# Kernel tuning notes

Hardware: AMD Instinct MI355X
Metric: run time of the kernel (lower is better)

## Reference

```python
import jax, jax.numpy as jnp
import numpy as np

SPATIAL = ((100, 134), (50, 67), (25, 34), (13, 17))
LEN = sum(h * w for h, w in SPATIAL)   # 17821
D, H, L, P = 384, 8, 4, 4
DH = D // H                            # 48
U = D // 3                             # unit_dim = 128
EPS = 1e-5


def _ln(x, g, b):
    m = jnp.mean(x, -1, keepdims=True)
    v = jnp.mean((x - m) ** 2, -1, keepdims=True)
    return (x - m) * jax.lax.rsqrt(v + EPS) * g + b


def _ffn(t, w1, b1, w2, b2, g, b):
    t2 = jax.nn.relu(t @ w1.T + b1) @ w2.T + b2
    return _ln(t + t2, g, b)


def _msda_core(value, loc, attn):
    # value [B,Lv,H,DH]; loc [B,Lq,H,L,P,2] normalized to [0,1]; attn [B,Lq,H,L,P]
    B = value.shape[0]
    Lq = loc.shape[1]
    out = jnp.zeros((B, H, Lq, DH), value.dtype)
    start = 0
    for lvl, (Hl, Wl) in enumerate(SPATIAL):
        n = Hl * Wl
        v = value[:, start:start + n].transpose(0, 2, 1, 3)        # [B,H,n,DH]
        # grid_sample(align_corners=False) semantics: pixel coord = loc*W - 0.5
        x = loc[:, :, :, lvl, :, 0] * Wl - 0.5                      # [B,Lq,H,P]
        y = loc[:, :, :, lvl, :, 1] * Hl - 0.5
        x0 = jnp.floor(x); y0 = jnp.floor(y)
        dx = x - x0; dy = y - y0
        x0i = x0.astype(jnp.int32); y0i = y0.astype(jnp.int32)
        acc = jnp.zeros((B, H, Lq, P, DH), value.dtype)
        corners = ((0, 0, (1 - dx) * (1 - dy)), (1, 0, dx * (1 - dy)),
                   (0, 1, (1 - dx) * dy), (1, 1, dx * dy))
        for ox, oy, w in corners:
            xi = x0i + ox; yi = y0i + oy
            valid = ((xi >= 0) & (xi < Wl) & (yi >= 0) & (yi < Hl)).astype(value.dtype)
            idx = jnp.clip(yi, 0, Hl - 1) * Wl + jnp.clip(xi, 0, Wl - 1)
            idx_t = idx.transpose(0, 2, 1, 3).reshape(B, H, Lq * P)
            g = jnp.take_along_axis(v, idx_t[..., None], axis=2).reshape(B, H, Lq, P, DH)
            acc = acc + g * (w * valid).transpose(0, 2, 1, 3)[..., None]
        out = out + (acc * attn[:, :, :, lvl].transpose(0, 2, 1, 3)[..., None]).sum(axis=3)
        start += n
    return out.transpose(0, 2, 1, 3).reshape(B, Lq, D)


def setup_inputs() -> dict:
    key = jax.random.key(0)
    ks = jax.random.split(key, 16)
    rn = lambda k, s, sc=1.0: jax.random.normal(k, s, jnp.float32) * sc
    inp = {}
    inp['src'] = rn(ks[0], (1, LEN, D))
    inp['space_query'] = rn(ks[1], (1, 1, 2 * U))
    inp['chann_query'] = rn(ks[2], (1, 1, 2 * U))
    inp['pos'] = rn(ks[3], (1, LEN, D))
    inp['reference_points'] = jax.random.uniform(ks[4], (1, LEN, L, 2), jnp.float32)
    inp['spatial_shapes'] = jnp.array(SPATIAL, jnp.int32)
    starts = np.cumsum([0] + [h * w for h, w in SPATIAL[:-1]])
    inp['level_start_index'] = jnp.array(starts, jnp.int32)
    inp['padding_mask'] = jnp.zeros((1, LEN), bool)
    # MSDeformAttn params (torch Linear convention: W is [out_features, in_features])
    inp['W_off'] = rn(ks[5], (H * L * P * 2, D), 0.01)
    inp['b_off'] = rn(ks[6], (H * L * P * 2,), 0.1)
    inp['W_attn'] = rn(ks[7], (H * L * P, D), D ** -0.5)
    inp['b_attn'] = jnp.zeros((H * L * P,), jnp.float32)
    inp['W_val'] = rn(ks[8], (D, D), D ** -0.5)
    inp['b_val'] = jnp.zeros((D,), jnp.float32)
    inp['W_out'] = rn(ks[9], (D, D), D ** -0.5)
    inp['b_out'] = jnp.zeros((D,), jnp.float32)
    # norm1_xy / norm1_zd
    inp['g1xy'] = jnp.ones((2 * U,), jnp.float32); inp['b1xy'] = jnp.zeros((2 * U,), jnp.float32)
    inp['g1zd'] = jnp.ones((U,), jnp.float32); inp['b1zd'] = jnp.zeros((U,), jnp.float32)
    # ffn_xy: Linear(2U,2U) -> relu -> Linear(2U,2U), residual + LN
    inp['fxy_w1'] = rn(ks[10], (2 * U, 2 * U), (2 * U) ** -0.5); inp['fxy_b1'] = jnp.zeros((2 * U,), jnp.float32)
    inp['fxy_w2'] = rn(ks[11], (2 * U, 2 * U), (2 * U) ** -0.5); inp['fxy_b2'] = jnp.zeros((2 * U,), jnp.float32)
    inp['fxy_g'] = jnp.ones((2 * U,), jnp.float32); inp['fxy_b'] = jnp.zeros((2 * U,), jnp.float32)
    # ffn_zd: Linear(U,U) -> relu -> Linear(U,U), residual + LN
    inp['fzd_w1'] = rn(ks[12], (U, U), U ** -0.5); inp['fzd_b1'] = jnp.zeros((U,), jnp.float32)
    inp['fzd_w2'] = rn(ks[13], (U, U), U ** -0.5); inp['fzd_b2'] = jnp.zeros((U,), jnp.float32)
    inp['fzd_g'] = jnp.ones((U,), jnp.float32); inp['fzd_b'] = jnp.zeros((U,), jnp.float32)
    return inp


def reference(src, space_query, chann_query, pos, reference_points, spatial_shapes,
              level_start_index, padding_mask,
              W_off, b_off, W_attn, b_attn, W_val, b_val, W_out, b_out,
              g1xy, b1xy, g1zd, b1zd,
              fxy_w1, fxy_b1, fxy_w2, fxy_b2, fxy_g, fxy_b,
              fzd_w1, fzd_b1, fzd_w2, fzd_b2, fzd_g, fzd_b):
    B, Lq, _ = src.shape
    q = src + pos                                        # with_pos_embed
    value = src @ W_val.T + b_val
    value = jnp.where(padding_mask[..., None], 0.0, value).reshape(B, Lq, H, DH)
    off = (q @ W_off.T + b_off).reshape(B, Lq, H, L, P, 2)
    attn = jax.nn.softmax((q @ W_attn.T + b_attn).reshape(B, Lq, H, L * P), -1)
    attn = attn.reshape(B, Lq, H, L, P)
    wh = jnp.array([[w, h] for h, w in SPATIAL], src.dtype)         # [L,2] as (W,H)
    loc = reference_points[:, :, None, :, None, :] + off / wh[None, None, None, :, None, :]
    src2 = _msda_core(value, loc, attn) @ W_out.T + b_out
    src_xy = _ln(src[..., :2 * U] + src2[..., :2 * U], g1xy, b1xy)
    src_zd = _ln(src[..., 2 * U:] + src2[..., 2 * U:], g1zd, b1zd)
    src_xy = _ffn(src_xy, fxy_w1, fxy_b1, fxy_w2, fxy_b2, fxy_g, fxy_b)
    src_zd = _ffn(src_zd, fzd_w1, fzd_b1, fzd_w2, fzd_b2, fzd_g, fzd_b)
    return jnp.concatenate([src_xy, src_zd], axis=-1)
```

## Files before the change

### kernel.cpp

```cpp
#include <hip/hip_runtime.h>
#include <math.h>

#define LEN 17821
#define DMODEL 384
#define NHEAD 8
#define DHEAD 48
#define WSZ (384 * 384)

typedef float floatx4 __attribute__((ext_vector_type(4)));
typedef short shortx8 __attribute__((ext_vector_type(8)));
typedef unsigned short ushort;

__device__ inline ushort f2bf(float f) {
    unsigned int u = __float_as_uint(f);
    u += 0x7FFFu + ((u >> 16) & 1u);
    return (ushort)(u >> 16);
}
__device__ inline float bf2f(ushort s) {
    return __uint_as_float(((unsigned int)s) << 16);
}

__device__ inline floatx4 mfma_bf16(shortx8 a, shortx8 b, floatx4 c) {
    return __builtin_amdgcn_mfma_f32_16x16x32_bf16(a, b, c, 0, 0, 0);
}

__global__ __launch_bounds__(256)
void prep_w(const float* __restrict__ Wval, const float* __restrict__ Woff,
            const float* __restrict__ Wattn, const float* __restrict__ Wout,
            const float* __restrict__ w1xy, const float* __restrict__ w1zd,
            const float* __restrict__ w2xy, const float* __restrict__ w2zd,
            ushort* __restrict__ wv, ushort* __restrict__ woa,
            ushort* __restrict__ wo, ushort* __restrict__ w1b,
            ushort* __restrict__ w2b) {
    int idx = blockIdx.x * 256 + threadIdx.x;
    if (idx >= WSZ) return;
    int job = blockIdx.y;
    float v; ushort* dst;
    if (job <= 1) {
        int n = idx / 384, k = idx - n * 384;
        if (job == 0) { v = Wval[idx]; dst = wv; }
        else {
            v = n < 256 ? Woff[n * 384 + k] : Wattn[(n - 256) * 384 + k];
            dst = woa;
        }
    } else {
        int e = idx & 7;
        int lane = (idx >> 3) & 63;
        int t = idx >> 9;
        int j = t % 6;
        int t2 = t / 6;
        int wv4 = t2 & 3;
        int ks = t2 >> 2;
        int l15 = lane & 15, quad = lane >> 4;
        int row = wv4 * 96 + j * 16 + l15;
        int k = ks * 32 + quad * 8 + e;
        if (job == 2) { v = Wout[row * 384 + k]; dst = wo; }
        else if (job == 3) {
            v = row < 256 ? (k < 256 ? w1xy[row * 256 + k] : 0.f)
                          : (k >= 256 ? w1zd[(row - 256) * 128 + (k - 256)] : 0.f);
            dst = w1b;
        } else {
            v = row < 256 ? (k < 256 ? w2xy[row * 256 + k] : 0.f)
                          : (k >= 256 ? w2zd[(row - 256) * 128 + (k - 256)] : 0.f);
            dst = w2b;
        }
    }
    dst[idx] = f2bf(v);
}

__global__ __launch_bounds__(384)
void prep_b(const float* __restrict__ boff, const float* __restrict__ battn,
            const float* __restrict__ b1xy, const float* __restrict__ b1zd,
            const float* __restrict__ b2xy, const float* __restrict__ b2zd,
            const float* __restrict__ g1xy, const float* __restrict__ be1xy,
            const float* __restrict__ g1zd, const float* __restrict__ be1zd,
            const float* __restrict__ g2xy, const float* __restrict__ be2xy,
            const float* __restrict__ g2zd, const float* __restrict__ be2zd,
            float* __restrict__ boa, float* __restrict__ b1c,
            float* __restrict__ b2c, float* __restrict__ l1g,
            float* __restrict__ l1b, float* __restrict__ l2g,
            float* __restrict__ l2b) {
    int i = threadIdx.x;
    bool lo = i < 256; int j = lo ? i : i - 256;
    boa[i] = lo ? boff[i] : battn[j];
    b1c[i] = lo ? b1xy[i] : b1zd[j];
    b2c[i] = lo ? b2xy[i] : b2zd[j];
    l1g[i] = lo ? g1xy[i] : g1zd[j];
    l1b[i] = lo ? be1xy[i] : be1zd[j];
    l2g[i] = lo ? g2xy[i] : g2zd[j];
    l2b[i] = lo ? be2xy[i] : be2zd[j];
}

__global__ __launch_bounds__(256)
void cvt_add(const float* __restrict__ src, const float* __restrict__ pos,
             ushort* __restrict__ src_bf, ushort* __restrict__ q_bf, int n8) {
    int i = blockIdx.x * 256 + threadIdx.x;
    if (i >= n8) return;
    float4 s0 = ((const float4*)src)[i * 2], s1 = ((const float4*)src)[i * 2 + 1];
    float4 p0 = ((const float4*)pos)[i * 2], p1 = ((const float4*)pos)[i * 2 + 1];
    shortx8 sb, qb;
    sb[0] = f2bf(s0.x); sb[1] = f2bf(s0.y); sb[2] = f2bf(s0.z); sb[3] = f2bf(s0.w);
    sb[4] = f2bf(s1.x); sb[5] = f2bf(s1.y); sb[6] = f2bf(s1.z); sb[7] = f2bf(s1.w);
    qb[0] = f2bf(s0.x + p0.x); qb[1] = f2bf(s0.y + p0.y);
    qb[2] = f2bf(s0.z + p0.z); qb[3] = f2bf(s0.w + p0.w);
    qb[4] = f2bf(s1.x + p1.x); qb[5] = f2bf(s1.y + p1.y);
    qb[6] = f2bf(s1.z + p1.z); qb[7] = f2bf(s1.w + p1.w);
    ((shortx8*)src_bf)[i] = sb;
    ((shortx8*)q_bf)[i] = qb;
}

#define TSV 128
#define LSTRIDE 40

__global__ __launch_bounds__(256)
void vq_gemm(const ushort* __restrict__ sbq, const ushort* __restrict__ qbq,
             const ushort* __restrict__ wv, const ushort* __restrict__ woa,
             const float* __restrict__ bval, const float* __restrict__ boa,
             ushort* __restrict__ vout, float* __restrict__ oaout) {
    __shared__ ushort As[TSV * LSTRIDE];
    __shared__ ushort Ws[TSV * LSTRIDE];
    bool job = blockIdx.x >= 3;
    int bx = job ? blockIdx.x - 3 : blockIdx.x;
    const ushort* A = job ? qbq : sbq;
    const ushort* W = job ? woa : wv;
    const float* bias = job ? boa : bval;
    int tid = threadIdx.x;
    int lane = tid & 63, wave = tid >> 6;
    int wr = (wave >> 1) * 64, wc = (wave & 1) * 64;
    int l15 = lane & 15, quad = lane >> 4;
    int srow = tid >> 1, shalf = tid & 1;
    int by = blockIdx.y;
    int garow = by * TSV + srow;
    bool avalid = garow < LEN;
    const ushort* ap = A + (size_t)(avalid ? garow : 0) * 384 + shalf * 16;
    const ushort* wp = W + (size_t)(bx * TSV + srow) * 384 + shalf * 16;
    ushort* as_dst = &As[srow * LSTRIDE + shalf * 16];
    ushort* ws_dst = &Ws[srow * LSTRIDE + shalf * 16];

    floatx4 acc[4][4];
    #pragma unroll
    for (int i = 0; i < 4; ++i)
        #pragma unroll
        for (int j = 0; j < 4; ++j)
            acc[i][j] = (floatx4){0.f, 0.f, 0.f, 0.f};

    shortx8 a0 = *(const shortx8*)(ap);
    shortx8 a1 = *(const shortx8*)(ap + 8);
    shortx8 w0 = *(const shortx8*)(wp);
    shortx8 w1 = *(const shortx8*)(wp + 8);

    for (int k0 = 0; k0 < 384; k0 += 32) {
        __syncthreads();
        *(shortx8*)(as_dst + 0) = a0;
        *(shortx8*)(as_dst + 8) = a1;
        *(shortx8*)(ws_dst + 0) = w0;
        *(shortx8*)(ws_dst + 8) = w1;
        __syncthreads();
        if (k0 + 32 < 384) {
            a0 = *(const shortx8*)(ap + k0 + 32);
            a1 = *(const shortx8*)(ap + k0 + 40);
            w0 = *(const shortx8*)(wp + k0 + 32);
            w1 = *(const shortx8*)(wp + k0 + 40);
        }
        shortx8 af[4], bfr[4];
        #pragma unroll
        for (int i = 0; i < 4; ++i)
            af[i] = *(shortx8*)&As[(wr + i * 16 + l15) * LSTRIDE + quad * 8];
        #pragma unroll
        for (int j = 0; j < 4; ++j)
            bfr[j] = *(shortx8*)&Ws[(wc + j * 16 + l15) * LSTRIDE + quad * 8];
        #pragma unroll
        for (int i = 0; i < 4; ++i)
            #pragma unroll
            for (int j = 0; j < 4; ++j)
                acc[i][j] = __builtin_amdgcn_mfma_f32_16x16x32_bf16(
                    af[i], bfr[j], acc[i][j], 0, 0, 0);
    }

    #pragma unroll
    for (int j = 0; j < 4; ++j) {
        int col = bx * TSV + wc + j * 16 + l15;
        float bv = bias[col];
        #pragma unroll
        for (int i = 0; i < 4; ++i) {
            #pragma unroll
            for (int r = 0; r < 4; ++r) {
                int row = by * TSV + wr + i * 16 + quad * 4 + r;
                if (row < LEN) {
                    float v = acc[i][j][r] + bv;
                    if (job) oaout[(size_t)row * 384 + col] = v;
                    else     vout[(size_t)row * 384 + col] = f2bf(v);
                }
            }
        }
    }
}

#define MTOK 8
__global__ __launch_bounds__(384)
void msda_v3(const ushort* __restrict__ value,
             const float* __restrict__ offattn,
             const float* __restrict__ refpts,
             ushort* __restrict__ out) {
    __shared__ int   sx0[MTOK * 128], sy0[MTOK * 128];
    __shared__ float sdx[MTOK * 128], sdy[MTOK * 128], saw[MTOK * 128];
    constexpr int Wi[4]  = {134, 67, 34, 17};
    constexpr int Hi[4]  = {100, 50, 25, 13};
    constexpr int STi[4] = {0, 13400, 16750, 17600};
    int t0 = blockIdx.x * MTOK;
    int tid = threadIdx.x;

    if (tid < MTOK * 8) {
        int ti = tid >> 3, h = tid & 7, t = t0 + ti;
        if (t < LEN) {
            const float* lg = offattn + (size_t)t * 384 + 256 + h * 16;
            float w[16], mx = -3.4e38f;
            #pragma unroll
            for (int s = 0; s < 16; ++s) { w[s] = lg[s]; mx = fmaxf(mx, w[s]); }
            float sum = 0.f;
            #pragma unroll
            for (int s = 0; s < 16; ++s) { w[s] = __expf(w[s] - mx); sum += w[s]; }
            float inv = 1.0f / sum;
            #pragma unroll
            for (int s = 0; s < 16; ++s) saw[ti * 128 + h * 16 + s] = w[s] * inv;
        }
    }
    for (int idx = tid; idx < MTOK * 128; idx += 384) {
        int ti = idx >> 7, rem = idx & 127, h = rem >> 4, p = rem & 15;
        int lvl = p >> 2, pp = p & 3;
        int t = t0 + ti;
        if (t < LEN) {
            float Wl = (float)Wi[lvl], Hl = (float)Hi[lvl];
            const float* op = offattn + (size_t)t * 384 + h * 32 + lvl * 8 + pp * 2;
            float ox = op[0], oy = op[1];
            float rx = refpts[(size_t)t * 8 + lvl * 2];
            float ry = refpts[(size_t)t * 8 + lvl * 2 + 1];
            float x = rx * Wl + ox - 0.5f;
            float y = ry * Hl + oy - 0.5f;
            float x0 = floorf(x), y0 = floorf(y);
            sx0[idx] = (int)x0; sy0[idx] = (int)y0;
            sdx[idx] = x - x0;  sdy[idx] = y - y0;
        }
    }
    __syncthreads();

    int ti = tid / 48;
    int r = tid - ti * 48;
    int h = r / 6;
    int c = r - h * 6;
    int t = t0 + ti;
    if (t >= LEN) return;
    const ushort* vb = value + h * DHEAD + c * 8;
    float a[8] = {};
    #pragma unroll
    for (int p = 0; p < 16; ++p) {
        const int lvl = p >> 2;
        const int Wl = Wi[lvl], Hl = Hi[lvl], st = STi[lvl];
        int base = ti * 128 + h * 16 + p;
        int x0 = sx0[base], y0 = sy0[base];
        float dx = sdx[base], dy = sdy[base], aw = saw[base];
        float cwv[4] = {(1.f - dx) * (1.f - dy), dx * (1.f - dy),
                        (1.f - dx) * dy, dx * dy};
        #pragma unroll
        for (int c2 = 0; c2 < 4; ++c2) {
            int xi = x0 + (c2 & 1), yi = y0 + (c2 >> 1);
            bool valid = (xi >= 0) & (xi < Wl) & (yi >= 0) & (yi < Hl);
            int xc = min(max(xi, 0), Wl - 1);
            int yc = min(max(yi, 0), Hl - 1);
            float s = valid ? aw * cwv[c2] : 0.f;
            shortx8 g = *(const shortx8*)(vb + (size_t)(st + yc * Wl + xc) * 384);
            #pragma unroll
            for (int k = 0; k < 8; ++k) a[k] += s * bf2f(g[k]);
        }
    }
    shortx8 o;
    #pragma unroll
    for (int k = 0; k < 8; ++k) o[k] = f2bf(a[k]);
    *(shortx8*)(out + (size_t)t * 384 + h * DHEAD + c * 8) = o;
}

#define MT 32
#define CST 392

#define GEMM384(WPTR)                                                         \
  {                                                                           \
    const ushort* wp_ = (WPTR) + wave * 3072 + lane * 8;                      \
    _Pragma("unroll")                                                         \
    for (int i_ = 0; i_ < 2; ++i_)                                            \
      _Pragma("unroll")                                                       \
      for (int j_ = 0; j_ < 6; ++j_) acc[i_][j_] = (floatx4){0.f,0.f,0.f,0.f};\
    shortx8 wcr[6][2], wnr[6][2];                                             \
    _Pragma("unroll")                                                         \
    for (int j_ = 0; j_ < 6; ++j_) {                                          \
      wcr[j_][0] = *(const shortx8*)(wp_ + j_ * 512);                         \
      wcr[j_][1] = *(const shortx8*)(wp_ + 12288 + j_ * 512);                 \
    }                                                                         \
    _Pragma("unroll")                                                         \
    for (int ks = 0; ks < 6; ++ks) {                                          \
      if (ks < 5) {                                                           \
        _Pragma("unroll")                                                     \
        for (int j_ = 0; j_ < 6; ++j_) {                                      \
          wnr[j_][0] = *(const shortx8*)(wp_ + (ks*2+2)*12288 + j_*512);      \
          wnr[j_][1] = *(const shortx8*)(wp_ + (ks*2+3)*12288 + j_*512);      \
        }                                                                     \
      }                                                                       \
      const int k0 = ks * 64;                                                 \
      shortx8 a0[2], a1[2];                                                   \
      a0[0] = *(shortx8*)&Cbuf[l15 * CST + k0 + quad * 8];                    \
      a0[1] = *(shortx8*)&Cbuf[l15 * CST + k0 + 32 + quad * 8];               \
      a1[0] = *(shortx8*)&Cbuf[(16 + l15) * CST + k0 + quad * 8];             \
      a1[1] = *(shortx8*)&Cbuf[(16 + l15) * CST + k0 + 32 + quad * 8];        \
      _Pragma("unroll")                                                       \
      for (int sk = 0; sk < 2; ++sk)                                          \
        _Pragma("unroll")                                                     \
        for (int j_ = 0; j_ < 6; ++j_) {                                      \
          acc[0][j_] = mfma_bf16(a0[sk], wcr[j_][sk], acc[0][j_]);            \
          acc[1][j_] = mfma_bf16(a1[sk], wcr[j_][sk], acc[1][j_]);            \
        }                                                                     \
      if (ks < 5) {                                                           \
        _Pragma("unroll")                                                     \
        for (int j_ = 0; j_ < 6; ++j_) {                                      \
          wcr[j_][0] = wnr[j_][0]; wcr[j_][1] = wnr[j_][1];                   \
        }                                                                     \
      }                                                                       \
    }                                                                         \
  }

__global__ __launch_bounds__(256, 4)
void mega_kernel(const ushort* __restrict__ Amsda, const float* __restrict__ src,
                 const ushort* __restrict__ Wo, const ushort* __restrict__ W1,
                 const ushort* __restrict__ W2,
                 const float* __restrict__ bo, const float* __restrict__ b1c,
                 const float* __restrict__ b2c,
                 const float* __restrict__ l1g, const float* __restrict__ l1b,
                 const float* __restrict__ l2g, const float* __restrict__ l2b,
                 float* __restrict__ h1f, float* __restrict__ outp) {
    __shared__ __align__(16) ushort Cbuf[MT * CST];
    __shared__ __align__(16) floatx4 pst4[MT * 8];
    __shared__ __align__(16) floatx4 lnf[MT];

    int tid = threadIdx.x;
    int lane = tid & 63, wave = tid >> 6;
    int l15 = lane & 15, quad = lane >> 4;
    int wcol = wave * 96;
    int by0 = blockIdx.x * MT;

    floatx4 acc[2][6];

    #pragma unroll
    for (int cix = 0; cix < 6; ++cix) {
        int idx = cix * 256 + tid;
        int row = idx / 48, c = idx - row * 48;
        int gr = min(by0 + row, LEN - 1);
        *(shortx8*)(Cbuf + row * CST + c * 8) =
            *(const shortx8*)(Amsda + (size_t)gr * 384 + c * 8);
    }
    __syncthreads();

    GEMM384(Wo);
    __syncthreads();

    #pragma unroll
    for (int j = 0; j < 6; ++j) {
        int col = wcol + j * 16 + l15;
        float bv = bo[col];
        #pragma unroll
        for (int i = 0; i < 2; ++i)
            #pragma unroll
            for (int rr = 0; rr < 4; ++rr) {
                int row = i * 16 + quad * 4 + rr;
                int gr = min(by0 + row, LEN - 1);
                float x = acc[i][j][rr] + bv + src[(size_t)gr * 384 + col];
                Cbuf[row * CST + col] = f2bf(x);
            }
    }
    __syncthreads();

    {
        int row = tid >> 3, part = tid & 7;
        float sx = 0.f, qx = 0.f, sz = 0.f, qz = 0.f;
        #pragma unroll
        for (int m = 0; m < 6; ++m) {
            int c0 = part * 48 + m * 8;
            shortx8 v = *(shortx8*)(Cbuf + row * CST + c0);
            float cs = 0.f, cq = 0.f;
            #pragma unroll
            for (int e = 0; e < 8; ++e) { float x = bf2f(v[e]); cs += x; cq += x * x; }
            if (c0 < 256) { sx += cs; qx += cq; } else { sz += cs; qz += cq; }
        }
        pst4[row * 8 + part] = (floatx4){sx, qx, sz, qz};
    }
    __syncthreads();
    if (tid < MT) {
        floatx4 s = (floatx4){0.f, 0.f, 0.f, 0.f};
        #pragma unroll
        for (int p = 0; p < 8; ++p) s += pst4[tid * 8 + p];
        float mx = s[0] / 256.f, vx = s[1] / 256.f - mx * mx;
        float mz = s[2] / 128.f, vz = s[3] / 128.f - mz * mz;
        lnf[tid] = (floatx4){mx, rsqrtf(vx + 1e-5f), mz, rsqrtf(vz + 1e-5f)};
    }
    __syncthreads();
    {
        int row = tid >> 3, part = tid & 7;
        int gr = by0 + row;
        floatx4 L = lnf[row];
        #pragma unroll
        for (int m = 0; m < 6; ++m) {
            int c0 = part * 48 + m * 8;
            bool isxy = c0 < 256;
            float mean = isxy ? L[0] : L[2];
            float inv  = isxy ? L[1] : L[3];
            shortx8 v = *(shortx8*)(Cbuf + row * CST + c0);
            float4 g0 = *(const float4*)(l1g + c0), g1 = *(const float4*)(l1g + c0 + 4);
            float4 e0 = *(const float4*)(l1b + c0), e1 = *(const float4*)(l1b + c0 + 4);
            float gg[8] = {g0.x, g0.y, g0.z, g0.w, g1.x, g1.y, g1.z, g1.w};
            float ee[8] = {e0.x, e0.y, e0.z, e0.w, e1.x, e1.y, e1.z, e1.w};
            float h[8];
            shortx8 hb;
            #pragma unroll
            for (int e = 0; e < 8; ++e) {
                h[e] = (bf2f(v[e]) - mean) * inv * gg[e] + ee[e];
                hb[e] = f2bf(h[e]);
            }
            *(shortx8*)(Cbuf + row * CST + c0) = hb;
            if (gr < LEN) {
                *(float4*)(h1f + (size_t)gr * 384 + c0)     = make_float4(h[0], h[1], h[2], h[3]);
                *(float4*)(h1f + (size_t)gr * 384 + c0 + 4) = make_float4(h[4], h[5], h[6], h[7]);
            }
        }
    }
    __syncthreads();

    GEMM384(W1);
    __syncthreads();
    #pragma unroll
    for (int j = 0; j < 6; ++j) {
        int col = wcol + j * 16 + l15;
        float bv = b1c[col];
        #pragma unroll
        for (int i = 0; i < 2; ++i)
            #pragma unroll
            for (int rr = 0; rr < 4; ++rr) {
                int row = i * 16 + quad * 4 + rr;
                Cbuf[row * CST + col] = f2bf(fmaxf(acc[i][j][rr] + bv, 0.f));
            }
    }
    __syncthreads();

    GEMM384(W2);
    __syncthreads();
    #pragma unroll
    for (int j = 0; j < 6; ++j) {
        int col = wcol + j * 16 + l15;
        float bv = b2c[col];
        #pragma unroll
        for (int i = 0; i < 2; ++i)
            #pragma unroll
            for (int rr = 0; rr < 4; ++rr) {
                int row = i * 16 + quad * 4 + rr;
                int gr = min(by0 + row, LEN - 1);
                float x = acc[i][j][rr] + bv + h1f[(size_t)gr * 384 + col];
                Cbuf[row * CST + col] = f2bf(x);
            }
    }
    __syncthreads();

    {
        int row = tid >> 3, part = tid & 7;
        float sx = 0.f, qx = 0.f, sz = 0.f, qz = 0.f;
        #pragma unroll
        for (int m = 0; m < 6; ++m) {
            int c0 = part * 48 + m * 8;
            shortx8 v = *(shortx8*)(Cbuf + row * CST + c0);
            float cs = 0.f, cq = 0.f;
            #pragma unroll
            for (int e = 0; e < 8; ++e) { float x = bf2f(v[e]); cs += x; cq += x * x; }
            if (c0 < 256) { sx += cs; qx += cq; } else { sz += cs; qz += cq; }
        }
        pst4[row * 8 + part] = (floatx4){sx, qx, sz, qz};
    }
    __syncthreads();
    if (tid < MT) {
        floatx4 s = (floatx4){0.f, 0.f, 0.f, 0.f};
        #pragma unroll
        for (int p = 0; p < 8; ++p) s += pst4[tid * 8 + p];
        float mx = s[0] / 256.f, vx = s[1] / 256.f - mx * mx;
        float mz = s[2] / 128.f, vz = s[3] / 128.f - mz * mz;
        lnf[tid] = (floatx4){mx, rsqrtf(vx + 1e-5f), mz, rsqrtf(vz + 1e-5f)};
    }
    __syncthreads();
    {
        int row = tid >> 3, part = tid & 7;
        int gr = by0 + row;
        if (gr < LEN) {
            floatx4 L = lnf[row];
            #pragma unroll
            for (int m = 0; m < 6; ++m) {
                int c0 = part * 48 + m * 8;
                bool isxy = c0 < 256;
                float mean = isxy ? L[0] : L[2];
                float inv  = isxy ? L[1] : L[3];
                shortx8 v = *(shortx8*)(Cbuf + row * CST + c0);
                float4 g0 = *(const float4*)(l2g + c0), g1 = *(const float4*)(l2g + c0 + 4);
                float4 e0 = *(const float4*)(l2b + c0), e1 = *(const float4*)(l2b + c0 + 4);
                float gg[8] = {g0.x, g0.y, g0.z, g0.w, g1.x, g1.y, g1.z, g1.w};
                float ee[8] = {e0.x, e0.y, e0.z, e0.w, e1.x, e1.y, e1.z, e1.w};
                float h[8];
                #pragma unroll
                for (int e = 0; e < 8; ++e)
                    h[e] = (bf2f(v[e]) - mean) * inv * gg[e] + ee[e];
                *(float4*)(outp + (size_t)gr * 384 + c0)     = make_float4(h[0], h[1], h[2], h[3]);
                *(float4*)(outp + (size_t)gr * 384 + c0 + 4) = make_float4(h[4], h[5], h[6], h[7]);
            }
        }
    }
}

extern "C" void kernel_launch(void* const* d_in, const int* in_sizes, int n_in,
                              void* d_out, int out_size, void* d_ws, size_t ws_size,
                              hipStream_t stream) {
    const float* src    = (const float*)d_in[0];
    const float* pos    = (const float*)d_in[3];
    const float* refpts = (const float*)d_in[4];
    const float* W_off  = (const float*)d_in[8];
    const float* b_off  = (const float*)d_in[9];
    const float* W_attn = (const float*)d_in[10];
    const float* b_attn = (const float*)d_in[11];
    const float* W_val  = (const float*)d_in[12];
    const float* b_val  = (const float*)d_in[13];
    const float* W_out  = (const float*)d_in[14];
    const float* b_out  = (const float*)d_in[15];
    const float* g1xy = (const float*)d_in[16]; const float* b1xy = (const float*)d_in[17];
    const float* g1zd = (const float*)d_in[18]; const float* b1zd = (const float*)d_in[19];
    const float* fxy_w1 = (const float*)d_in[20]; const float* fxy_b1 = (const float*)d_in[21];
    const float* fxy_w2 = (const float*)d_in[22]; const float* fxy_b2 = (const float*)d_in[23];
    const float* fxy_g  = (const float*)d_in[24]; const float* fxy_b  = (const float*)d_in[25];
    const float* fzd_w1 = (const float*)d_in[26]; const float* fzd_b1 = (const float*)d_in[27];
    const float* fzd_w2 = (const float*)d_in[28]; const float* fzd_b2 = (const float*)d_in[29];
    const float* fzd_g  = (const float*)d_in[30]; const float* fzd_b  = (const float*)d_in[31];

    float* out = (float*)d_out;
    size_t Rn = (size_t)LEN * DMODEL;

    float* f0 = (float*)d_ws;
    ushort* sb = (ushort*)(f0 + Rn);
    ushort* s0 = sb;
    ushort* s1 = sb + Rn;
    ushort* s2 = sb + 2 * Rn;
    ushort* s3 = sb + 3 * Rn;
    ushort* wv  = sb + 4 * Rn;
    ushort* woa = wv + WSZ;
    ushort* wo  = woa + WSZ;
    ushort* w1b = wo + WSZ;
    ushort* w2b = w1b + WSZ;
    float* bp = (float*)(w2b + WSZ);
    float* boa = bp;        float* b1c = bp + 384;  float* b2c = bp + 768;
    float* l1g = bp + 1152; float* l1b = bp + 1536;
    float* l2g = bp + 1920; float* l2b = bp + 2304;

    prep_w<<<dim3((WSZ + 255) / 256, 5), 256, 0, stream>>>(
        W_val, W_off, W_attn, W_out, fxy_w1, fzd_w1, fxy_w2, fzd_w2,
        wv, woa, wo, w1b, w2b);
    prep_b<<<1, 384, 0, stream>>>(b_off, b_attn, fxy_b1, fzd_b1, fxy_b2, fzd_b2,
                                  g1xy, b1xy, g1zd, b1zd, fxy_g, fxy_b, fzd_g, fzd_b,
                                  boa, b1c, b2c, l1g, l1b, l2g, l2b);

    int n8 = (int)(Rn / 8);
    cvt_add<<<(n8 + 255) / 256, 256, 0, stream>>>(src, pos, s0, s1, n8);

    vq_gemm<<<dim3(6, (LEN + TSV - 1) / TSV), 256, 0, stream>>>(
        s0, s1, wv, woa, b_val, boa, s2, f0);

    msda_v3<<<(LEN + MTOK - 1) / MTOK, 384, 0, stream>>>(s2, f0, refpts, s3);

    mega_kernel<<<(LEN + MT - 1) / MT, 256, 0, stream>>>(
        s3, src, wo, w1b, w2b, b_out, b1c, b2c,
        l1g, l1b, l2g, l2b, f0, out);
}
```

Baseline: 334.0 us.

## Restructure value/offset GEMM to stage full A rows in LDS with register-fed weights

The value and offset/attention projection GEMM now loads a 64-row strip of the full 384-wide activations into shared memory once. Each wave streams pre-swizzled bf16 weight fragments straight from global memory into registers with one-step prefetch, so the per-k-step double barrier is gone. It reuses the MFMA-fragment weight layout already used by the mega kernel and covers all 384 output columns per block. The mega kernel's launch bound also drops from 4 to 2 blocks per SM, giving more registers at the cost of occupancy. Weights are now read from global or L2 by every block instead of being tiled through LDS.

```diff
diff --git a/kernel.cpp b/kernel.cpp
--- a/kernel.cpp
+++ b/kernel.cpp
@@ -35,35 +35,30 @@
     int idx = blockIdx.x * 256 + threadIdx.x;
     if (idx >= WSZ) return;
     int job = blockIdx.y;
+    int e = idx & 7;
+    int lane = (idx >> 3) & 63;
+    int t = idx >> 9;
+    int j = t % 6;
+    int t2 = t / 6;
+    int wv4 = t2 & 3;
+    int hs = t2 >> 2;
+    int l15 = lane & 15, quad = lane >> 4;
+    int row = wv4 * 96 + j * 16 + l15;
+    int k = hs * 32 + quad * 8 + e;
     float v; ushort* dst;
-    if (job <= 1) {
-        int n = idx / 384, k = idx - n * 384;
-        if (job == 0) { v = Wval[idx]; dst = wv; }
-        else {
-            v = n < 256 ? Woff[n * 384 + k] : Wattn[(n - 256) * 384 + k];
-            dst = woa;
-        }
+    if (job == 0) { v = Wval[row * 384 + k]; dst = wv; }
+    else if (job == 1) {
+        v = row < 256 ? Woff[row * 384 + k] : Wattn[(row - 256) * 384 + k];
+        dst = woa;
+    } else if (job == 2) { v = Wout[row * 384 + k]; dst = wo; }
+    else if (job == 3) {
+        v = row < 256 ? (k < 256 ? w1xy[row * 256 + k] : 0.f)
+                      : (k >= 256 ? w1zd[(row - 256) * 128 + (k - 256)] : 0.f);
+        dst = w1b;
     } else {
-        int e = idx & 7;
-        int lane = (idx >> 3) & 63;
-        int t = idx >> 9;
-        int j = t % 6;
-        int t2 = t / 6;
-        int wv4 = t2 & 3;
-        int ks = t2 >> 2;
-        int l15 = lane & 15, quad = lane >> 4;
-        int row = wv4 * 96 + j * 16 + l15;
-        int k = ks * 32 + quad * 8 + e;
-        if (job == 2) { v = Wout[row * 384 + k]; dst = wo; }
-        else if (job == 3) {
-            v = row < 256 ? (k < 256 ? w1xy[row * 256 + k] : 0.f)
-                          : (k >= 256 ? w1zd[(row - 256) * 128 + (k - 256)] : 0.f);
-            dst = w1b;
-        } else {
-            v = row < 256 ? (k < 256 ? w2xy[row * 256 + k] : 0.f)
-                          : (k >= 256 ? w2zd[(row - 256) * 128 + (k - 256)] : 0.f);
-            dst = w2b;
-        }
+        v = row < 256 ? (k < 256 ? w2xy[row * 256 + k] : 0.f)
+                      : (k >= 256 ? w2zd[(row - 256) * 128 + (k - 256)] : 0.f);
+        dst = w2b;
     }
     dst[idx] = f2bf(v);
 }
@@ -109,87 +104,81 @@
     ((shortx8*)q_bf)[i] = qb;
 }
 
-#define TSV 128
-#define LSTRIDE 40
-
-__global__ __launch_bounds__(256)
+#define VMT 64
+#define VCST 392
+
+__global__ __launch_bounds__(256, 2)
 void vq_gemm(const ushort* __restrict__ sbq, const ushort* __restrict__ qbq,
              const ushort* __restrict__ wv, const ushort* __restrict__ woa,
              const float* __restrict__ bval, const float* __restrict__ boa,
              ushort* __restrict__ vout, float* __restrict__ oaout) {
-    __shared__ ushort As[TSV * LSTRIDE];
-    __shared__ ushort Ws[TSV * LSTRIDE];
-    bool job = blockIdx.x >= 3;
-    int bx = job ? blockIdx.x - 3 : blockIdx.x;
+    __shared__ __align__(16) ushort Abuf[VMT * VCST];
+    bool job = blockIdx.y != 0;
     const ushort* A = job ? qbq : sbq;
-    const ushort* W = job ? woa : wv;
+    const ushort* Wp = job ? woa : wv;
     const float* bias = job ? boa : bval;
     int tid = threadIdx.x;
     int lane = tid & 63, wave = tid >> 6;
-    int wr = (wave >> 1) * 64, wc = (wave & 1) * 64;
     int l15 = lane & 15, quad = lane >> 4;
-    int srow = tid >> 1, shalf = tid & 1;
-    int by = blockIdx.y;
-    int garow = by * TSV + srow;
-    bool avalid = garow < LEN;
-    const ushort* ap = A + (size_t)(avalid ? garow : 0) * 384 + shalf * 16;
-    const ushort* wp = W + (size_t)(bx * TSV + srow) * 384 + shalf * 16;
-    ushort* as_dst = &As[srow * LSTRIDE + shalf * 16];
-    ushort* ws_dst = &Ws[srow * LSTRIDE + shalf * 16];
-
-    floatx4 acc[4][4];
+    int wcol = wave * 96;
+    int by0 = blockIdx.x * VMT;
+
+    #pragma unroll
+    for (int it = 0; it < 12; ++it) {
+        int idx = it * 256 + tid;
+        int row = idx / 48, c = idx - row * 48;
+        int gr = min(by0 + row, LEN - 1);
+        *(shortx8*)(Abuf + row * VCST + c * 8) =
+            *(const shortx8*)(A + (size_t)gr * 384 + c * 8);
+    }
+    __syncthreads();
+
+    floatx4 acc[4][6];
     #pragma unroll
     for (int i = 0; i < 4; ++i)
         #pragma unroll
-        for (int j = 0; j < 4; ++j)
-            acc[i][j] = (floatx4){0.f, 0.f, 0.f, 0.f};
-
-    shortx8 a0 = *(const shortx8*)(ap);
-    shortx8 a1 = *(const shortx8*)(ap + 8);
-    shortx8 w0 = *(const shortx8*)(wp);
-    shortx8 w1 = *(const shortx8*)(wp + 8);
-
-    for (int k0 = 0; k0 < 384; k0 += 32) {
-        __syncthreads();
-        *(shortx8*)(as_dst + 0) = a0;
-        *(shortx8*)(as_dst + 8) = a1;
-        *(shortx8*)(ws_dst + 0) = w0;
-        *(shortx8*)(ws_dst + 8) = w1;
-        __syncthreads();
-        if (k0 + 32 < 384) {
-            a0 = *(const shortx8*)(ap + k0 + 32);
-            a1 = *(const shortx8*)(ap + k0 + 40);
-            w0 = *(const shortx8*)(wp + k0 + 32);
-            w1 = *(const shortx8*)(wp + k0 + 40);
-        }
-        shortx8 af[4], bfr[4];
+        for (int j = 0; j < 6; ++j) acc[i][j] = (floatx4){0.f, 0.f, 0.f, 0.f};
+
+    const ushort* wp_ = Wp + wave * 3072 + lane * 8;
+    shortx8 wcr[6], wnr[6];
+    #pragma unroll
+    for (int j = 0; j < 6; ++j)
+        wcr[j] = *(const shortx8*)(wp_ + j * 512);
+    #pragma unroll
+    for (int hs = 0; hs < 12; ++hs) {
+        if (hs < 11) {
+            #pragma unroll
+            for (int j = 0; j < 6; ++j)
+                wnr[j] = *(const shortx8*)(wp_ + (hs + 1) * 12288 + j * 512);
+        }
+        shortx8 a[4];
         #pragma unroll
         for (int i = 0; i < 4; ++i)
-            af[i] = *(shortx8*)&As[(wr + i * 16 + l15) * LSTRIDE + quad * 8];
-        #pragma unroll
-        for (int j = 0; j < 4; ++j)
-            bfr[j] = *(shortx8*)&Ws[(wc + j * 16 + l15) * LSTRIDE + quad * 8];
-        #pragma unroll
-        for (int i = 0; i < 4; ++i)
-            #pragma unroll
-            for (int j = 0; j < 4; ++j)
-                acc[i][j] = __builtin_amdgcn_mfma_f32_16x16x32_bf16(
-                    af[i], bfr[j], acc[i][j], 0, 0, 0);
-    }
-
-    #pragma unroll
-    for (int j = 0; j < 4; ++j) {
-        int col = bx * TSV + wc + j * 16 + l15;
+            a[i] = *(shortx8*)&Abuf[(i * 16 + l15) * VCST + hs * 32 + quad * 8];
+        #pragma unroll
+        for (int j = 0; j < 6; ++j)
+            #pragma unroll
+            for (int i = 0; i < 4; ++i)
+                acc[i][j] = mfma_bf16(a[i], wcr[j], acc[i][j]);
+        if (hs < 11) {
+            #pragma unroll
+            for (int j = 0; j < 6; ++j) wcr[j] = wnr[j];
+        }
+    }
+
+    #pragma unroll
+    for (int j = 0; j < 6; ++j) {
+        int col = wcol + j * 16 + l15;
         float bv = bias[col];
         #pragma unroll
         for (int i = 0; i < 4; ++i) {
             #pragma unroll
             for (int r = 0; r < 4; ++r) {
-                int row = by * TSV + wr + i * 16 + quad * 4 + r;
-                if (row < LEN) {
+                int gr = by0 + i * 16 + quad * 4 + r;
+                if (gr < LEN) {
                     float v = acc[i][j][r] + bv;
-                    if (job) oaout[(size_t)row * 384 + col] = v;
-                    else     vout[(size_t)row * 384 + col] = f2bf(v);
+                    if (job) oaout[(size_t)gr * 384 + col] = v;
+                    else     vout[(size_t)gr * 384 + col] = f2bf(v);
                 }
             }
         }
@@ -326,7 +315,7 @@
     }                                                                         \
   }
 
-__global__ __launch_bounds__(256, 4)
+__global__ __launch_bounds__(256, 2)
 void mega_kernel(const ushort* __restrict__ Amsda, const float* __restrict__ src,
                  const ushort* __restrict__ Wo, const ushort* __restrict__ W1,
                  const ushort* __restrict__ W2,
@@ -568,7 +557,7 @@
     int n8 = (int)(Rn / 8);
     cvt_add<<<(n8 + 255) / 256, 256, 0, stream>>>(src, pos, s0, s1, n8);
 
-    vq_gemm<<<dim3(6, (LEN + TSV - 1) / TSV), 256, 0, stream>>>(
+    vq_gemm<<<dim3((LEN + VMT - 1) / VMT, 2), 256, 0, stream>>>(
         s0, s1, wv, woa, b_val, boa, s2, f0);
 
     msda_v3<<<(LEN + MTOK - 1) / MTOK, 384, 0, stream>>>(s2, f0, refpts, s3);
```

After: 359.6 us. 1.08x slower.
